# Performance work log

Hardware: AMD Instinct MI355X
Metric: run time of the kernel (lower is better)

The kernel has to match this reference:

```python
import jax, jax.numpy as jnp
import numpy as np

IN_DIM, OUT_DIM = 4096, 11008
NUM_SUBDIM, KS = 1376, 256
DS = OUT_DIM // NUM_SUBDIM  # 8
BATCH = 32


def setup_inputs() -> dict:
    key = jax.random.key(0)
    k1, k2, k3, k4 = jax.random.split(key, 4)
    x = jax.random.normal(k1, (BATCH, IN_DIM), dtype=jnp.float32)
    vectors = jax.random.normal(k2, (NUM_SUBDIM, KS, DS), dtype=jnp.float32)
    bias = jax.random.normal(k3, (OUT_DIM,), dtype=jnp.float32)
    indexes = jax.random.randint(k4, (IN_DIM, NUM_SUBDIM), 0, KS, dtype=jnp.int64)
    return {"x": x, "vectors": vectors, "bias": bias, "indexes": indexes}


def reference(x, vectors, bias, indexes):
    in_dim, num_subdim = indexes.shape
    ds = vectors.shape[-1]
    # PQ dequant: gather codewords per (row, subspace) -> [in_dim, num_subdim, Ds]
    # vectors[d, indexes[i, d]] via broadcast of arange(num_subdim) against indexes.
    dims = jnp.arange(num_subdim)
    weight = vectors[dims, indexes].reshape(in_dim, num_subdim * ds)  # [in_dim, out_dim]
    return x @ weight + bias
```

## Files before the change

### kernel.cpp

```cpp
#include <hip/hip_runtime.h>

#define IN_DIM  4096
#define OUT_DIM 11008
#define NSUB    1376
#define KSQ     256
#define DSUB    8
#define BATCH   32

#define DTILE   8
#define NTILE   64
#define KC      64
#define KSPLIT  8
#define KPB     (IN_DIM / KSPLIT)
#define NCHUNK  4
#define NBLK    (OUT_DIM / NTILE)
#define NBLKP   176
#define NPX     (NBLKP / 8)
#define GRID_MAIN (NBLKP * KSPLIT)

typedef unsigned short ushort_t;
typedef unsigned int   uint_t;
typedef unsigned char  uchar_t;
typedef __attribute__((ext_vector_type(8))) short bf16x8;
typedef __attribute__((ext_vector_type(4))) float f32x4;

#define VEC_N    (NSUB * KSQ * DSUB)
#define XBF_OFF  (VEC_N * 2)
#define IDXT_OFF (XBF_OFF + BATCH * IN_DIM * 2)
#define SLAB_OFF (IDXT_OFF + NSUB * IN_DIM)
#define PREP_V   (VEC_N / 2)
#define PREP_X   (BATCH * IN_DIM / 2)
#define PREP_N   (PREP_V + PREP_X)
#define PACK_BLK (PREP_N / 256)
#define IDXT_BLK ((IN_DIM / 128) * (NSUB / 32))

__device__ __forceinline__ ushort_t f2bf(float f) {
    union { float f; uint_t u; } a; a.f = f;
    uint_t u = a.u;
    u += 0x7fffu + ((u >> 16) & 1u);
    return (ushort_t)(u >> 16);
}

__global__ __launch_bounds__(256) void pq_prep(
    const float* __restrict__ x, const float* __restrict__ vecs,
    const int* __restrict__ idx,
    uint_t* __restrict__ vbf, uint_t* __restrict__ xbf,
    uchar_t* __restrict__ idx8T)
{
    __shared__ uchar_t sT[32][144];
    const int t = threadIdx.x;

    if (blockIdx.x < PACK_BLK) {
        int tid = blockIdx.x * 256 + t;
        if (tid < PREP_V) {
            float2 v = ((const float2*)vecs)[tid];
            vbf[tid] = (uint_t)f2bf(v.x) | ((uint_t)f2bf(v.y) << 16);
        } else {
            int i = tid - PREP_V;
            float2 v = ((const float2*)x)[i];
            xbf[i] = (uint_t)f2bf(v.x) | ((uint_t)f2bf(v.y) << 16);
        }
        return;
    }

    const int bid = blockIdx.x - PACK_BLK;
    const int k0 = (bid & 31) * 128, d0 = (bid >> 5) * 32;
    #pragma unroll
    for (int p = 0; p < 16; ++p) {
        int f = p * 256 + t;
        int kk = f >> 5, dd = f & 31;
        sT[dd][kk] = (uchar_t)idx[(size_t)(k0 + kk) * NSUB + d0 + dd];
    }
    __syncthreads();
    int dd = t >> 3, seg = t & 7;
    uint4 v = *(const uint4*)&sT[dd][seg * 16];
    *(uint4*)&idx8T[(size_t)(d0 + dd) * IN_DIM + k0 + seg * 16] = v;
}

__global__ __launch_bounds__(256, 4) void pq_main(
    const ushort_t* __restrict__ xbfu, const uint4* __restrict__ vbf4,
    const uchar_t* __restrict__ idx8T, float* __restrict__ slab)
{
    __shared__ uint4  sV4[4 * 512];
    __shared__ uint_t sW32[4 * 16 * 32];

    const int id  = blockIdx.x;
    const int xcd = id & 7;
    const int s   = id >> 3;
    const int nblk = xcd * NPX + (s % NPX);
    const int kblk = s / NPX;
    if (nblk >= NBLK) return;

    const int t    = threadIdx.x;
    const int w    = t >> 6;
    const int lane = t & 63;
    const int d0   = nblk * DTILE;
    const int kbase = kblk * KPB;

    const int l15 = lane & 15;
    const int l4  = lane >> 4;
    const int dl  = lane >> 5;
    const int q   = lane & 31;

    {
        const size_t src0 = (size_t)(d0 + w * 2) * KSQ;
        #pragma unroll
        for (int h = 0; h < 2; ++h) {
            uint4 vst[4];
            #pragma unroll
            for (int p = 0; p < 4; ++p)
                vst[p] = vbf4[src0 + (h * 4 + p) * 64 + lane];
            #pragma unroll
            for (int p = 0; p < 4; ++p)
                sV4[w * 512 + (h * 4 + p) * 64 + lane] = vst[p];
        }
    }

    f32x4 acc[2];
    acc[0] = (f32x4)0.0f; acc[1] = (f32x4)0.0f;

    const uchar_t* idxrow = idx8T + (size_t)(d0 + w * 2 + dl) * IN_DIM + kbase;
    const int vbase = w * 512 + dl * 256;
    const int Rbase = (w * 16 + dl * 8) * 32;

    #pragma unroll
    for (int h = 0; h < 2; ++h) {
        const int kh = kbase + h * 256;

        bf16x8 A[2][8];
        #pragma unroll
        for (int mt = 0; mt < 2; ++mt)
            #pragma unroll
            for (int kk = 0; kk < 8; ++kk)
                A[mt][kk] = *(const bf16x8*)
                    &xbfu[(size_t)(mt * 16 + l15) * IN_DIM + kh + kk * 32 + l4 * 8];

        uint_t bb[NCHUNK];
        #pragma unroll
        for (int c = 0; c < NCHUNK; ++c)
            bb[c] = *(const ushort_t*)&idxrow[h * 256 + c * KC + q * 2];

        __builtin_amdgcn_sched_barrier(0);

        #pragma unroll
        for (int c = 0; c < NCHUNK; ++c) {
            uint4 g0 = sV4[vbase + (bb[c] & 255)];
            uint4 g1 = sV4[vbase + (bb[c] >> 8)];

            #pragma unroll
            for (int j = 0; j < 8; ++j) {
                const uint_t sel = (j & 1) ? 0x07060302u : 0x05040100u;
                uint_t a0 = (j >> 1) == 0 ? g0.x : (j >> 1) == 1 ? g0.y : (j >> 1) == 2 ? g0.z : g0.w;
                uint_t a1 = (j >> 1) == 0 ? g1.x : (j >> 1) == 1 ? g1.y : (j >> 1) == 2 ? g1.z : g1.w;
                uint_t wv = __builtin_amdgcn_perm(a1, a0, sel);
                int dw = ((((q >> 2) ^ j) << 2) | (q & 3));
                sW32[Rbase + j * 32 + dw] = wv;
            }

            #pragma unroll
            for (int kq = 0; kq < 2; ++kq) {
                int u16 = (kq * 4 + l4) ^ (l15 & 7);
                bf16x8 B = *(const bf16x8*)
                    ((const char*)sW32 + (w * 16 + l15) * 128 + u16 * 16);
                #pragma unroll
                for (int mt = 0; mt < 2; ++mt)
                    acc[mt] = __builtin_amdgcn_mfma_f32_16x16x32_bf16(
                        A[mt][c * 2 + kq], B, acc[mt], 0, 0, 0);
            }
        }
    }

    float* sl = slab + (size_t)kblk * BATCH * OUT_DIM;
    const int col = nblk * NTILE + w * 16 + l15;
    #pragma unroll
    for (int mt = 0; mt < 2; ++mt)
        #pragma unroll
        for (int r = 0; r < 4; ++r)
            sl[(size_t)(mt * 16 + l4 * 4 + r) * OUT_DIM + col] = acc[mt][r];
}

__global__ __launch_bounds__(256) void pq_reduce(
    const float* __restrict__ slab, const float* __restrict__ bias,
    float* __restrict__ out)
{
    int i = blockIdx.x * 256 + threadIdx.x;
    int m = i / (OUT_DIM / 4), n4 = i - m * (OUT_DIM / 4);
    float4 s = ((const float4*)bias)[n4];
    #pragma unroll
    for (int kb = 0; kb < KSPLIT; ++kb) {
        float4 v = ((const float4*)slab)[(size_t)(kb * BATCH + m) * (OUT_DIM / 4) + n4];
        s.x += v.x; s.y += v.y; s.z += v.z; s.w += v.w;
    }
    ((float4*)out)[(size_t)m * (OUT_DIM / 4) + n4] = s;
}

extern "C" void kernel_launch(void* const* d_in, const int* in_sizes, int n_in,
                              void* d_out, int out_size, void* d_ws, size_t ws_size,
                              hipStream_t stream) {
    const float* x    = (const float*)d_in[0];
    const float* vecs = (const float*)d_in[1];
    const float* bias = (const float*)d_in[2];
    const int*   idx  = (const int*)d_in[3];
    float* out = (float*)d_out;

    uint_t*  vbf   = (uint_t*)d_ws;
    uint_t*  xbf   = (uint_t*)((char*)d_ws + XBF_OFF);
    uchar_t* idx8T = (uchar_t*)((char*)d_ws + IDXT_OFF);
    float*   slab  = (float*)((char*)d_ws + SLAB_OFF);

    pq_prep<<<PACK_BLK + IDXT_BLK, 256, 0, stream>>>(x, vecs, idx, vbf, xbf, idx8T);
    pq_main<<<GRID_MAIN, 256, 0, stream>>>(
        (const ushort_t*)xbf, (const uint4*)vbf, idx8T, slab);
    pq_reduce<<<(BATCH * OUT_DIM / 4) / 256, 256, 0, stream>>>(slab, bias, out);
}
```

Before: 113.2 us.

## Fuse bf16 conversion into main kernel and double KSPLIT with gather prefetch

Drops the separate pass that turned x and the codebook vectors into bf16 in workspace. The main kernel now reads fp32 directly and converts in registers. KSPLIT goes from 8 to 16 so each block covers half as much K in a single pass, and the codebook gather for the next chunk is software-prefetched. This removes a full read/write pass over the ~11MB codebook, but each block now re-converts its codebook slice, and twice as many blocks repeat that load. The partial-sum slab also doubles, which raises reduce traffic.

```diff
diff --git a/kernel.cpp b/kernel.cpp
--- a/kernel.cpp
+++ b/kernel.cpp
@@ -10,9 +10,9 @@
 #define DTILE   8
 #define NTILE   64
 #define KC      64
-#define KSPLIT  8
+#define KSPLIT  16
 #define KPB     (IN_DIM / KSPLIT)
-#define NCHUNK  4
+#define NCHUNK  (KPB / KC)
 #define NBLK    (OUT_DIM / NTILE)
 #define NBLKP   176
 #define NPX     (NBLKP / 8)
@@ -24,14 +24,8 @@
 typedef __attribute__((ext_vector_type(8))) short bf16x8;
 typedef __attribute__((ext_vector_type(4))) float f32x4;
 
-#define VEC_N    (NSUB * KSQ * DSUB)
-#define XBF_OFF  (VEC_N * 2)
-#define IDXT_OFF (XBF_OFF + BATCH * IN_DIM * 2)
-#define SLAB_OFF (IDXT_OFF + NSUB * IN_DIM)
-#define PREP_V   (VEC_N / 2)
-#define PREP_X   (BATCH * IN_DIM / 2)
-#define PREP_N   (PREP_V + PREP_X)
-#define PACK_BLK (PREP_N / 256)
+#define IDXT_OFF 0
+#define SLAB_OFF (NSUB * IN_DIM)
 #define IDXT_BLK ((IN_DIM / 128) * (NSUB / 32))
 
 __device__ __forceinline__ ushort_t f2bf(float f) {
@@ -40,31 +34,16 @@
     u += 0x7fffu + ((u >> 16) & 1u);
     return (ushort_t)(u >> 16);
 }
+__device__ __forceinline__ uint_t pack2(float lo, float hi) {
+    return (uint_t)f2bf(lo) | ((uint_t)f2bf(hi) << 16);
+}
 
 __global__ __launch_bounds__(256) void pq_prep(
-    const float* __restrict__ x, const float* __restrict__ vecs,
-    const int* __restrict__ idx,
-    uint_t* __restrict__ vbf, uint_t* __restrict__ xbf,
-    uchar_t* __restrict__ idx8T)
+    const int* __restrict__ idx, uchar_t* __restrict__ idx8T)
 {
     __shared__ uchar_t sT[32][144];
     const int t = threadIdx.x;
-
-    if (blockIdx.x < PACK_BLK) {
-        int tid = blockIdx.x * 256 + t;
-        if (tid < PREP_V) {
-            float2 v = ((const float2*)vecs)[tid];
-            vbf[tid] = (uint_t)f2bf(v.x) | ((uint_t)f2bf(v.y) << 16);
-        } else {
-            int i = tid - PREP_V;
-            float2 v = ((const float2*)x)[i];
-            xbf[i] = (uint_t)f2bf(v.x) | ((uint_t)f2bf(v.y) << 16);
-        }
-        return;
-    }
-
-    const int bid = blockIdx.x - PACK_BLK;
-    const int k0 = (bid & 31) * 128, d0 = (bid >> 5) * 32;
+    const int k0 = (blockIdx.x & 31) * 128, d0 = (blockIdx.x >> 5) * 32;
     #pragma unroll
     for (int p = 0; p < 16; ++p) {
         int f = p * 256 + t;
@@ -78,7 +57,7 @@
 }
 
 __global__ __launch_bounds__(256, 4) void pq_main(
-    const ushort_t* __restrict__ xbfu, const uint4* __restrict__ vbf4,
+    const float* __restrict__ xf, const float4* __restrict__ vf4,
     const uchar_t* __restrict__ idx8T, float* __restrict__ slab)
 {
     __shared__ uint4  sV4[4 * 512];
@@ -103,71 +82,78 @@
     const int q   = lane & 31;
 
     {
-        const size_t src0 = (size_t)(d0 + w * 2) * KSQ;
+        const float4* src4 = vf4 + (size_t)(d0 + w * 2) * (KSQ * DSUB / 4);
         #pragma unroll
-        for (int h = 0; h < 2; ++h) {
-            uint4 vst[4];
-            #pragma unroll
-            for (int p = 0; p < 4; ++p)
-                vst[p] = vbf4[src0 + (h * 4 + p) * 64 + lane];
-            #pragma unroll
-            for (int p = 0; p < 4; ++p)
-                sV4[w * 512 + (h * 4 + p) * 64 + lane] = vst[p];
+        for (int p = 0; p < 8; ++p) {
+            float4 v0 = src4[(p * 64 + lane) * 2];
+            float4 v1 = src4[(p * 64 + lane) * 2 + 1];
+            uint4 o;
+            o.x = pack2(v0.x, v0.y); o.y = pack2(v0.z, v0.w);
+            o.z = pack2(v1.x, v1.y); o.w = pack2(v1.z, v1.w);
+            sV4[w * 512 + p * 64 + lane] = o;
         }
     }
+
+    bf16x8 A[2][8];
+    #pragma unroll
+    for (int mt = 0; mt < 2; ++mt)
+        #pragma unroll
+        for (int kk = 0; kk < 8; ++kk) {
+            const float* ap = &xf[(size_t)(mt * 16 + l15) * IN_DIM + kbase + kk * 32 + l4 * 8];
+            float4 a0 = *(const float4*)ap;
+            float4 a1 = *(const float4*)(ap + 4);
+            union { bf16x8 v; uint4 u; } cv;
+            cv.u.x = pack2(a0.x, a0.y); cv.u.y = pack2(a0.z, a0.w);
+            cv.u.z = pack2(a1.x, a1.y); cv.u.w = pack2(a1.z, a1.w);
+            A[mt][kk] = cv.v;
+        }
+
+    const uchar_t* idxrow = idx8T + (size_t)(d0 + w * 2 + dl) * IN_DIM + kbase;
+    uint_t bb[NCHUNK];
+    #pragma unroll
+    for (int c = 0; c < NCHUNK; ++c)
+        bb[c] = *(const ushort_t*)&idxrow[c * KC + q * 2];
+
+    __builtin_amdgcn_sched_barrier(0);
 
     f32x4 acc[2];
     acc[0] = (f32x4)0.0f; acc[1] = (f32x4)0.0f;
 
-    const uchar_t* idxrow = idx8T + (size_t)(d0 + w * 2 + dl) * IN_DIM + kbase;
     const int vbase = w * 512 + dl * 256;
     const int Rbase = (w * 16 + dl * 8) * 32;
 
+    uint4 g0 = sV4[vbase + (bb[0] & 255)];
+    uint4 g1 = sV4[vbase + (bb[0] >> 8)];
+
     #pragma unroll
-    for (int h = 0; h < 2; ++h) {
-        const int kh = kbase + h * 256;
+    for (int c = 0; c < NCHUNK; ++c) {
+        #pragma unroll
+        for (int j = 0; j < 8; ++j) {
+            const uint_t sel = (j & 1) ? 0x07060302u : 0x05040100u;
+            uint_t a0 = (j >> 1) == 0 ? g0.x : (j >> 1) == 1 ? g0.y : (j >> 1) == 2 ? g0.z : g0.w;
+            uint_t a1 = (j >> 1) == 0 ? g1.x : (j >> 1) == 1 ? g1.y : (j >> 1) == 2 ? g1.z : g1.w;
+            uint_t wv = __builtin_amdgcn_perm(a1, a0, sel);
+            int dw = ((((q >> 2) ^ j) << 2) | (q & 3));
+            sW32[Rbase + j * 32 + dw] = wv;
+        }
 
-        bf16x8 A[2][8];
-        #pragma unroll
-        for (int mt = 0; mt < 2; ++mt)
-            #pragma unroll
-            for (int kk = 0; kk < 8; ++kk)
-                A[mt][kk] = *(const bf16x8*)
-                    &xbfu[(size_t)(mt * 16 + l15) * IN_DIM + kh + kk * 32 + l4 * 8];
-
-        uint_t bb[NCHUNK];
-        #pragma unroll
-        for (int c = 0; c < NCHUNK; ++c)
-            bb[c] = *(const ushort_t*)&idxrow[h * 256 + c * KC + q * 2];
-
-        __builtin_amdgcn_sched_barrier(0);
+        uint4 n0 = g0, n1 = g1;
+        if (c + 1 < NCHUNK) {
+            n0 = sV4[vbase + (bb[c + 1] & 255)];
+            n1 = sV4[vbase + (bb[c + 1] >> 8)];
+        }
 
         #pragma unroll
-        for (int c = 0; c < NCHUNK; ++c) {
-            uint4 g0 = sV4[vbase + (bb[c] & 255)];
-            uint4 g1 = sV4[vbase + (bb[c] >> 8)];
-
+        for (int kq = 0; kq < 2; ++kq) {
+            int u16 = (kq * 4 + l4) ^ (l15 & 7);
+            bf16x8 B = *(const bf16x8*)
+                ((const char*)sW32 + (w * 16 + l15) * 128 + u16 * 16);
             #pragma unroll
-            for (int j = 0; j < 8; ++j) {
-                const uint_t sel = (j & 1) ? 0x07060302u : 0x05040100u;
-                uint_t a0 = (j >> 1) == 0 ? g0.x : (j >> 1) == 1 ? g0.y : (j >> 1) == 2 ? g0.z : g0.w;
-                uint_t a1 = (j >> 1) == 0 ? g1.x : (j >> 1) == 1 ? g1.y : (j >> 1) == 2 ? g1.z : g1.w;
-                uint_t wv = __builtin_amdgcn_perm(a1, a0, sel);
-                int dw = ((((q >> 2) ^ j) << 2) | (q & 3));
-                sW32[Rbase + j * 32 + dw] = wv;
-            }
-
-            #pragma unroll
-            for (int kq = 0; kq < 2; ++kq) {
-                int u16 = (kq * 4 + l4) ^ (l15 & 7);
-                bf16x8 B = *(const bf16x8*)
-                    ((const char*)sW32 + (w * 16 + l15) * 128 + u16 * 16);
-                #pragma unroll
-                for (int mt = 0; mt < 2; ++mt)
-                    acc[mt] = __builtin_amdgcn_mfma_f32_16x16x32_bf16(
-                        A[mt][c * 2 + kq], B, acc[mt], 0, 0, 0);
-            }
+            for (int mt = 0; mt < 2; ++mt)
+                acc[mt] = __builtin_amdgcn_mfma_f32_16x16x32_bf16(
+                    A[mt][c * 2 + kq], B, acc[mt], 0, 0, 0);
         }
+        g0 = n0; g1 = n1;
     }
 
     float* sl = slab + (size_t)kblk * BATCH * OUT_DIM;
@@ -203,13 +189,11 @@
     const int*   idx  = (const int*)d_in[3];
     float* out = (float*)d_out;
 
-    uint_t*  vbf   = (uint_t*)d_ws;
-    uint_t*  xbf   = (uint_t*)((char*)d_ws + XBF_OFF);
     uchar_t* idx8T = (uchar_t*)((char*)d_ws + IDXT_OFF);
     float*   slab  = (float*)((char*)d_ws + SLAB_OFF);
 
-    pq_prep<<<PACK_BLK + IDXT_BLK, 256, 0, stream>>>(x, vecs, idx, vbf, xbf, idx8T);
+    pq_prep<<<IDXT_BLK, 256, 0, stream>>>(idx, idx8T);
     pq_main<<<GRID_MAIN, 256, 0, stream>>>(
-        (const ushort_t*)xbf, (const uint4*)vbf, idx8T, slab);
+        x, (const float4*)vecs, idx8T, slab);
     pq_reduce<<<(BATCH * OUT_DIM / 4) / 256, 256, 0, stream>>>(slab, bias, out);
 }
```

Measured after the change: 133.9 us. 18.3% more time.

## Double K-split and prefetch all operands before a software-pipelined gather loop

Applied to the files above, without the earlier changes.

KSPLIT goes from 8 to 16, so each block covers 256 K values in a single pass. The global loads for codewords, x fragments and indices are all issued up front, before the LDS stores. Empty asm pins keep those values resident in registers. The inner loop prefetches the next chunk's codeword gathers from LDS while the current chunk is permuted and fed to the MFMAs, aiming to hide global and LDS latency. The cost is twice the partial-sum slab traffic in the reduce kernel, twice as many blocks, and more register pressure.

```diff
diff --git a/kernel.cpp b/kernel.cpp
--- a/kernel.cpp
+++ b/kernel.cpp
@@ -10,9 +10,9 @@
 #define DTILE   8
 #define NTILE   64
 #define KC      64
-#define KSPLIT  8
+#define KSPLIT  16
 #define KPB     (IN_DIM / KSPLIT)
-#define NCHUNK  4
+#define NCHUNK  (KPB / KC)
 #define NBLK    (OUT_DIM / NTILE)
 #define NBLKP   176
 #define NPX     (NBLKP / 8)
@@ -41,6 +41,14 @@
     return (ushort_t)(u >> 16);
 }
 
+__device__ __forceinline__ void pin4(uint4& x) {
+    asm volatile("" : "+v"(x.x), "+v"(x.y), "+v"(x.z), "+v"(x.w));
+}
+__device__ __forceinline__ void pin1(uint_t& x) { asm volatile("" : "+v"(x)); }
+__device__ __forceinline__ bf16x8 as_bf16x8(uint4 u) {
+    union { uint4 u; bf16x8 v; } c; c.u = u; return c.v;
+}
+
 __global__ __launch_bounds__(256) void pq_prep(
     const float* __restrict__ x, const float* __restrict__ vecs,
     const int* __restrict__ idx,
@@ -102,72 +110,81 @@
     const int dl  = lane >> 5;
     const int q   = lane & 31;
 
+    uint4 vst[8];
     {
         const size_t src0 = (size_t)(d0 + w * 2) * KSQ;
         #pragma unroll
-        for (int h = 0; h < 2; ++h) {
-            uint4 vst[4];
-            #pragma unroll
-            for (int p = 0; p < 4; ++p)
-                vst[p] = vbf4[src0 + (h * 4 + p) * 64 + lane];
-            #pragma unroll
-            for (int p = 0; p < 4; ++p)
-                sV4[w * 512 + (h * 4 + p) * 64 + lane] = vst[p];
-        }
-    }
+        for (int p = 0; p < 8; ++p)
+            vst[p] = vbf4[src0 + p * 64 + lane];
+    }
+
+    uint4 A[2][8];
+    #pragma unroll
+    for (int mt = 0; mt < 2; ++mt)
+        #pragma unroll
+        for (int kk = 0; kk < 8; ++kk)
+            A[mt][kk] = *(const uint4*)
+                &xbfu[(size_t)(mt * 16 + l15) * IN_DIM + kbase + kk * 32 + l4 * 8];
+
+    const uchar_t* idxrow = idx8T + (size_t)(d0 + w * 2 + dl) * IN_DIM + kbase;
+    uint_t bb[NCHUNK];
+    #pragma unroll
+    for (int c = 0; c < NCHUNK; ++c)
+        bb[c] = *(const ushort_t*)&idxrow[c * KC + q * 2];
+
+    #pragma unroll
+    for (int p = 0; p < 8; ++p)
+        sV4[w * 512 + p * 64 + lane] = vst[p];
+
+    #pragma unroll
+    for (int mt = 0; mt < 2; ++mt)
+        #pragma unroll
+        for (int kk = 0; kk < 8; ++kk)
+            pin4(A[mt][kk]);
+    #pragma unroll
+    for (int c = 0; c < NCHUNK; ++c)
+        pin1(bb[c]);
+
+    __builtin_amdgcn_sched_barrier(0);
 
     f32x4 acc[2];
     acc[0] = (f32x4)0.0f; acc[1] = (f32x4)0.0f;
 
-    const uchar_t* idxrow = idx8T + (size_t)(d0 + w * 2 + dl) * IN_DIM + kbase;
     const int vbase = w * 512 + dl * 256;
     const int Rbase = (w * 16 + dl * 8) * 32;
 
-    #pragma unroll
-    for (int h = 0; h < 2; ++h) {
-        const int kh = kbase + h * 256;
-
-        bf16x8 A[2][8];
-        #pragma unroll
-        for (int mt = 0; mt < 2; ++mt)
+    uint4 g0 = sV4[vbase + (bb[0] & 255)];
+    uint4 g1 = sV4[vbase + (bb[0] >> 8)];
+
+    #pragma unroll
+    for (int c = 0; c < NCHUNK; ++c) {
+        #pragma unroll
+        for (int j = 0; j < 8; ++j) {
+            const uint_t sel = (j & 1) ? 0x07060302u : 0x05040100u;
+            uint_t a0 = (j >> 1) == 0 ? g0.x : (j >> 1) == 1 ? g0.y : (j >> 1) == 2 ? g0.z : g0.w;
+            uint_t a1 = (j >> 1) == 0 ? g1.x : (j >> 1) == 1 ? g1.y : (j >> 1) == 2 ? g1.z : g1.w;
+            uint_t wv = __builtin_amdgcn_perm(a1, a0, sel);
+            int dw = ((((q >> 2) ^ j) << 2) | (q & 3));
+            sW32[Rbase + j * 32 + dw] = wv;
+        }
+
+        uint4 n0 = g0, n1 = g1;
+        if (c + 1 < NCHUNK) {
+            n0 = sV4[vbase + (bb[c + 1] & 255)];
+            n1 = sV4[vbase + (bb[c + 1] >> 8)];
+        }
+
+        #pragma unroll
+        for (int kq = 0; kq < 2; ++kq) {
+            int u16 = (kq * 4 + l4) ^ (l15 & 7);
+            bf16x8 B = *(const bf16x8*)
+                ((const char*)sW32 + (w * 16 + l15) * 128 + u16 * 16);
             #pragma unroll
-            for (int kk = 0; kk < 8; ++kk)
-                A[mt][kk] = *(const bf16x8*)
-                    &xbfu[(size_t)(mt * 16 + l15) * IN_DIM + kh + kk * 32 + l4 * 8];
-
-        uint_t bb[NCHUNK];
-        #pragma unroll
-        for (int c = 0; c < NCHUNK; ++c)
-            bb[c] = *(const ushort_t*)&idxrow[h * 256 + c * KC + q * 2];
-
-        __builtin_amdgcn_sched_barrier(0);
-
-        #pragma unroll
-        for (int c = 0; c < NCHUNK; ++c) {
-            uint4 g0 = sV4[vbase + (bb[c] & 255)];
-            uint4 g1 = sV4[vbase + (bb[c] >> 8)];
-
-            #pragma unroll
-            for (int j = 0; j < 8; ++j) {
-                const uint_t sel = (j & 1) ? 0x07060302u : 0x05040100u;
-                uint_t a0 = (j >> 1) == 0 ? g0.x : (j >> 1) == 1 ? g0.y : (j >> 1) == 2 ? g0.z : g0.w;
-                uint_t a1 = (j >> 1) == 0 ? g1.x : (j >> 1) == 1 ? g1.y : (j >> 1) == 2 ? g1.z : g1.w;
-                uint_t wv = __builtin_amdgcn_perm(a1, a0, sel);
-                int dw = ((((q >> 2) ^ j) << 2) | (q & 3));
-                sW32[Rbase + j * 32 + dw] = wv;
-            }
-
-            #pragma unroll
-            for (int kq = 0; kq < 2; ++kq) {
-                int u16 = (kq * 4 + l4) ^ (l15 & 7);
-                bf16x8 B = *(const bf16x8*)
-                    ((const char*)sW32 + (w * 16 + l15) * 128 + u16 * 16);
-                #pragma unroll
-                for (int mt = 0; mt < 2; ++mt)
-                    acc[mt] = __builtin_amdgcn_mfma_f32_16x16x32_bf16(
-                        A[mt][c * 2 + kq], B, acc[mt], 0, 0, 0);
-            }
-        }
+            for (int mt = 0; mt < 2; ++mt)
+                acc[mt] = __builtin_amdgcn_mfma_f32_16x16x32_bf16(
+                    as_bf16x8(A[mt][c * 2 + kq]), B, acc[mt], 0, 0, 0);
+        }
+        g0 = n0; g1 = n1;
     }
 
     float* sl = slab + (size_t)kblk * BATCH * OUT_DIM;
```

After: 114.3 us. Within noise of the previous version (+1.0%).
